# Optimization experiments

Hardware: AMD Instinct MI355X
Metric: run time of the kernel (lower is better)

Reference implementation:

```python
import jax, jax.numpy as jnp
import numpy as np

B, N, C, H, D, CS, CZ = 2, 512, 768, 16, 48, 384, 128  # batch, tokens, c_token, heads, head_dim, c_s, c_pair


def _ln(x, w=None, b=None, eps=1e-5):
    m = jnp.mean(x, axis=-1, keepdims=True)
    v = jnp.mean(jnp.square(x - m), axis=-1, keepdims=True)
    y = (x - m) * jax.lax.rsqrt(v + eps)
    if w is not None:
        y = y * w
    if b is not None:
        y = y + b
    return y


def setup_inputs() -> dict:
    key = jax.random.key(0)
    ks = jax.random.split(key, 16)
    s = 0.02
    return {
        "a_i": jax.random.normal(ks[0], (B, N, C), jnp.float32),
        "s_i": jax.random.normal(ks[1], (B, N, CS), jnp.float32),
        "z_ij": jax.random.normal(ks[2], (B, N, N, CZ), jnp.float32),
        "beta_ij": jax.random.normal(ks[3], (B, N, N), jnp.float32),
        # MHA projections (CustomAttention: q has bias; k, v, g, o have no bias)
        "Wq": jax.random.normal(ks[4], (C, C), jnp.float32) * s,
        "bq": jnp.zeros((C,), jnp.float32),
        "Wk": jax.random.normal(ks[5], (C, C), jnp.float32) * s,
        "Wv": jax.random.normal(ks[6], (C, C), jnp.float32) * s,
        "Wg": jax.random.normal(ks[7], (C, C), jnp.float32) * s,
        "Wo": jax.random.normal(ks[8], (C, C), jnp.float32) * s,
        # AdaLN: LN1 no affine; LN2 weight only; linear (bias) + linear_no_bias
        "ada_ln2_w": jnp.ones((CS,), jnp.float32),
        "ada_Wl": jax.random.normal(ks[9], (C, CS), jnp.float32) * s,
        "ada_bl": jnp.zeros((C,), jnp.float32),
        "ada_Wnb": jax.random.normal(ks[10], (C, CS), jnp.float32) * s,
        # pair-bias path
        "lnz_w": jnp.ones((CZ,), jnp.float32),
        "lnz_b": jnp.zeros((CZ,), jnp.float32),
        "Wz": jax.random.normal(ks[11], (H, CZ), jnp.float32) * s,
        # output gating from s_i (bias initialized to -2.0)
        "Wgs": jax.random.normal(ks[12], (C, CS), jnp.float32) * s,
        "bgs": jnp.full((C,), -2.0, jnp.float32),
    }


def reference(a_i, s_i, z_ij, beta_ij, Wq, bq, Wk, Wv, Wg, Wo,
              ada_ln2_w, ada_Wl, ada_bl, ada_Wnb, lnz_w, lnz_b, Wz, Wgs, bgs):
    b, n, c = a_i.shape
    # AdaLN conditioning
    a = _ln(a_i)                                   # [B,N,C], no affine
    s = _ln(s_i, ada_ln2_w)                        # [B,N,CS], weight only
    a = jax.nn.sigmoid(s @ ada_Wl.T + ada_bl) * a + s @ ada_Wnb.T
    # pair bias: LN(z) -> per-head logits -> [B,H,N,N]
    zb = _ln(z_ij, lnz_w, lnz_b) @ Wz.T            # [B,N,N,H]
    bias = jnp.transpose(zb, (0, 3, 1, 2)) + beta_ij[:, None, :, :]
    # multi-head attention with additive bias
    q = (a @ Wq.T + bq).reshape(b, n, H, D) / jnp.sqrt(jnp.asarray(D, a.dtype))
    k = (a @ Wk.T).reshape(b, n, H, D)
    v = (a @ Wv.T).reshape(b, n, H, D)
    scores = jnp.einsum("bqhd,bkhd->bhqk", q, k) + bias
    attn = jax.nn.softmax(scores, axis=-1)
    o = jnp.einsum("bhqk,bkhd->bqhd", attn, v)     # [B,N,H,D]
    g = jax.nn.sigmoid((a @ Wg.T).reshape(b, n, H, D))
    o = (g * o).reshape(b, n, c) @ Wo.T
    # final gating from raw s_i
    return jax.nn.sigmoid(s_i @ Wgs.T + bgs) * o
```

## Files before the change

kernel.cpp:

```cpp
#include <hip/hip_runtime.h>
#include <hip/hip_bf16.h>

#define NB 2
#define NN 512
#define CC 768
#define NH 16
#define DD 48
#define CS 384
#define CZ 128

__device__ inline float2 wave_reduce_sum2(float s, float q) {
  #pragma unroll
  for (int off = 32; off > 0; off >>= 1) {
    s += __shfl_xor(s, off);
    q += __shfl_xor(q, off);
  }
  return make_float2(s, q);
}

__device__ inline float sigmoidf_(float x) { return 1.f / (1.f + __expf(-x)); }

__global__ __launch_bounds__(256) void k_ln(
    const float* __restrict__ a_i, const float* __restrict__ s_i,
    const float* __restrict__ ln2w,
    float* __restrict__ aln, float* __restrict__ sln) {
  int r = blockIdx.x, t = threadIdx.x;
  int lane = t & 63, w = t >> 6;
  __shared__ float red[2][4];

  const float* ar = a_i + (size_t)r * CC;
  float x0 = ar[t], x1 = ar[t + 256], x2 = ar[t + 512];
  float s = x0 + x1 + x2, sq = x0 * x0 + x1 * x1 + x2 * x2;
  float2 rs = wave_reduce_sum2(s, sq);
  if (lane == 0) { red[0][w] = rs.x; red[1][w] = rs.y; }
  __syncthreads();
  float S = red[0][0] + red[0][1] + red[0][2] + red[0][3];
  float SQ = red[1][0] + red[1][1] + red[1][2] + red[1][3];
  float mean = S * (1.f / CC);
  float var = SQ * (1.f / CC) - mean * mean;
  float rstd = rsqrtf(var + 1e-5f);
  float* alr = aln + (size_t)r * CC;
  alr[t] = (x0 - mean) * rstd;
  alr[t + 256] = (x1 - mean) * rstd;
  alr[t + 512] = (x2 - mean) * rstd;

  const float* sr = s_i + (size_t)r * CS;
  float y0 = sr[t];
  float y1 = (t < 128) ? sr[256 + t] : 0.f;
  float s2 = y0 + y1, sq2 = y0 * y0 + y1 * y1;
  float2 rs2 = wave_reduce_sum2(s2, sq2);
  __syncthreads();
  if (lane == 0) { red[0][w] = rs2.x; red[1][w] = rs2.y; }
  __syncthreads();
  float S2 = red[0][0] + red[0][1] + red[0][2] + red[0][3];
  float SQ2 = red[1][0] + red[1][1] + red[1][2] + red[1][3];
  float mean2 = S2 * (1.f / CS);
  float var2 = SQ2 * (1.f / CS) - mean2 * mean2;
  float rstd2 = rsqrtf(var2 + 1e-5f);
  float* slr = sln + (size_t)r * CS;
  slr[t] = (y0 - mean2) * rstd2 * ln2w[t];
  if (t < 128) slr[256 + t] = (y1 - mean2) * rstd2 * ln2w[256 + t];
}

__global__ __launch_bounds__(256) void k_adaln(
    const float* __restrict__ sln, const float* __restrict__ aln,
    const float* __restrict__ Wl, const float* __restrict__ bl,
    const float* __restrict__ Wnb, float* __restrict__ acond) {
  __shared__ __align__(16) float As[16][36], B1[16][68], B2[16][68];
  int cb = blockIdx.x * 64, rb = blockIdx.y * 32;
  int t = threadIdx.x, tr = t >> 4, tc = t & 15;
  int lk = t & 15, lr = t >> 4;
  float acc1[2][4] = {}, acc2[2][4] = {};
  for (int kb = 0; kb < CS; kb += 16) {
    #pragma unroll
    for (int i = 0; i < 2; ++i) {
      int row = lr + i * 16;
      As[lk][row] = sln[(size_t)(rb + row) * CS + kb + lk];
    }
    #pragma unroll
    for (int i = 0; i < 4; ++i) {
      int row = lr + i * 16;
      B1[lk][row] = Wl[(size_t)(cb + row) * CS + kb + lk];
      B2[lk][row] = Wnb[(size_t)(cb + row) * CS + kb + lk];
    }
    __syncthreads();
    #pragma unroll
    for (int k = 0; k < 16; ++k) {
      float2 av = ((const float2*)&As[k][0])[tr];
      float4 b1v = ((const float4*)&B1[k][0])[tc];
      float4 b2v = ((const float4*)&B2[k][0])[tc];
      float a[2] = {av.x, av.y};
      float b1a[4] = {b1v.x, b1v.y, b1v.z, b1v.w};
      float b2a[4] = {b2v.x, b2v.y, b2v.z, b2v.w};
      #pragma unroll
      for (int i = 0; i < 2; ++i)
        #pragma unroll
        for (int j = 0; j < 4; ++j) {
          acc1[i][j] += a[i] * b1a[j];
          acc2[i][j] += a[i] * b2a[j];
        }
    }
    __syncthreads();
  }
  #pragma unroll
  for (int i = 0; i < 2; ++i) {
    int r = rb + tr * 2 + i;
    #pragma unroll
    for (int j = 0; j < 4; ++j) {
      int c = cb + tc * 4 + j;
      float sig = sigmoidf_(acc1[i][j] + bl[c]);
      acond[(size_t)r * CC + c] = sig * aln[(size_t)r * CC + c] + acc2[i][j];
    }
  }
}

__global__ __launch_bounds__(256) void k_qkvg(
    const float* __restrict__ acond,
    const float* __restrict__ Wq, const float* __restrict__ bq,
    const float* __restrict__ Wk, const float* __restrict__ Wv,
    const float* __restrict__ Wg,
    float* __restrict__ qo, float* __restrict__ ko,
    float* __restrict__ vo, float* __restrict__ go) {
  __shared__ __align__(16) float As[16][68], Bs[16][68];
  int zid = blockIdx.z;
  const float* W = (zid == 0) ? Wq : (zid == 1) ? Wk : (zid == 2) ? Wv : Wg;
  int cb = blockIdx.x * 64, rb = blockIdx.y * 64;
  int t = threadIdx.x, tr = t >> 4, tc = t & 15;
  int lk = t & 15, lr = t >> 4;
  float acc[4][4] = {};
  for (int kb = 0; kb < CC; kb += 16) {
    #pragma unroll
    for (int i = 0; i < 4; ++i) {
      int row = lr + i * 16;
      As[lk][row] = acond[(size_t)(rb + row) * CC + kb + lk];
      Bs[lk][row] = W[(size_t)(cb + row) * CC + kb + lk];
    }
    __syncthreads();
    #pragma unroll
    for (int k = 0; k < 16; ++k) {
      float4 av = ((const float4*)&As[k][0])[tr];
      float4 bv = ((const float4*)&Bs[k][0])[tc];
      float a[4] = {av.x, av.y, av.z, av.w};
      float bb[4] = {bv.x, bv.y, bv.z, bv.w};
      #pragma unroll
      for (int i = 0; i < 4; ++i)
        #pragma unroll
        for (int j = 0; j < 4; ++j) acc[i][j] += a[i] * bb[j];
    }
    __syncthreads();
  }
  const float qscale = 0.14433756729740643f;
  #pragma unroll
  for (int i = 0; i < 4; ++i) {
    int r = rb + tr * 4 + i;
    #pragma unroll
    for (int j = 0; j < 4; ++j) {
      int c = cb + tc * 4 + j;
      size_t o = (size_t)r * CC + c;
      if (zid == 0)      qo[o] = (acc[i][j] + bq[c]) * qscale;
      else if (zid == 1) ko[o] = acc[i][j];
      else if (zid == 2) vo[o] = acc[i][j];
      else               go[o] = sigmoidf_(acc[i][j]);
    }
  }
}

__global__ __launch_bounds__(256) void k_wzprep(
    const float* __restrict__ lnzw, const float* __restrict__ lnzb,
    const float* __restrict__ Wz, float* __restrict__ Wzp,
    float* __restrict__ TK) {
  int t = threadIdx.x;
  for (int idx = t; idx < NH * CZ; idx += 256)
    Wzp[idx] = lnzw[idx & (CZ - 1)] * Wz[idx];
  if (t < 32) {
    int h = t & 15;
    const float* wr = Wz + (size_t)h * CZ;
    const float* coef = (t < 16) ? lnzw : lnzb;
    float acc = 0.f;
    for (int c = 0; c < CZ; ++c) acc += coef[c] * wr[c];
    TK[(t < 16) ? h : 16 + h] = acc;
  }
}

__global__ __launch_bounds__(256) void k_pairbias(
    const float* __restrict__ z, const float* __restrict__ beta,
    const float* __restrict__ Wzp, const float* __restrict__ TK,
    float* __restrict__ bias) {
  __shared__ __align__(16) float zs[256 * 32];
  int blk = blockIdx.x;
  int jh = blk & 1, i = (blk >> 1) & (NN - 1), b = blk >> 10;
  int t = threadIdx.x;
  int j = jh * 256 + t;

  const float* zbase = z + ((size_t)(b * NN + i) * NN + jh * 256) * CZ;
  const float4* Wzp4 = (const float4*)Wzp;
  float S[16];
  #pragma unroll
  for (int h = 0; h < 16; ++h) S[h] = 0.f;
  float sum = 0.f, sq = 0.f;

  int srow = t >> 3;
  int ss = t & 7;

  for (int ch = 0; ch < 4; ++ch) {
    __syncthreads();
    #pragma unroll
    for (int p = 0; p < 8; ++p) {
      int r = p * 32 + srow;
      float4 v = *(const float4*)(zbase + (size_t)r * CZ + ch * 32 + ss * 4);
      *(float4*)&zs[r * 32 + ((ss ^ (r & 7)) << 2)] = v;
    }
    __syncthreads();
    #pragma unroll
    for (int s = 0; s < 8; ++s) {
      float4 zv = *(const float4*)&zs[t * 32 + ((s ^ (t & 7)) << 2)];
      sum += (zv.x + zv.y) + (zv.z + zv.w);
      sq += zv.x * zv.x + zv.y * zv.y + zv.z * zv.z + zv.w * zv.w;
      #pragma unroll
      for (int h = 0; h < 16; ++h) {
        float4 wv = Wzp4[h * 32 + ch * 8 + s];
        S[h] += zv.x * wv.x + zv.y * wv.y + zv.z * wv.z + zv.w * wv.w;
      }
    }
  }
  float mean = sum * (1.f / CZ);
  float var = fmaxf(sq * (1.f / CZ) - mean * mean, 0.f);
  float rstd = rsqrtf(var + 1e-5f);
  float bet = beta[((size_t)(b * NN + i)) * NN + j];
  size_t obase = (((size_t)b * NH) * NN + i) * NN + j;
  #pragma unroll
  for (int h = 0; h < 16; ++h) {
    bias[obase + (size_t)h * NN * NN] =
        rstd * (S[h] - mean * TK[h]) + TK[16 + h] + bet;
  }
}

__global__ __launch_bounds__(256) void k_attn(
    const float* __restrict__ q, const float* __restrict__ k,
    const float* __restrict__ v, const float* __restrict__ g,
    const float* __restrict__ bias, float* __restrict__ go_out) {
  __shared__ __align__(16) float qs[32][49];
  __shared__ __align__(16) float ks[64][49];
  __shared__ __align__(16) float vs[64][49];
  __shared__ __align__(16) float ps[32][65];
  __shared__ __align__(16) float bs[32][65];
  __shared__ float mrow[32], lrow[32], crow[32];
  int blk = blockIdx.x;
  int it = blk & 15, h = (blk >> 4) & 15, b = blk >> 8;
  int ibase = it * 32;
  int t = threadIdx.x;
  int tr = t >> 4, tc = t & 15;
  int td = t & 15;
  int sr = t >> 3, sl = t & 7;

  for (int idx = t; idx < 32 * 48; idx += 256) {
    int r = idx / 48, c = idx % 48;
    qs[r][c] = q[((size_t)(b * NN) + ibase + r) * CC + h * DD + c];
  }
  if (t < 32) { mrow[t] = -1e30f; lrow[t] = 0.f; }
  float acc[2][3] = {};
  const size_t bh = (size_t)b * NH + h;

  for (int jb = 0; jb < NN; jb += 64) {
    __syncthreads();
    for (int idx = t; idx < 64 * 48; idx += 256) {
      int r = idx / 48, c = idx % 48;
      size_t src = ((size_t)(b * NN) + jb + r) * CC + h * DD + c;
      ks[r][c] = k[src];
      vs[r][c] = v[src];
    }
    for (int idx = t; idx < 32 * 64; idx += 256) {
      int r = idx >> 6, c = idx & 63;
      bs[r][c] = bias[(bh * NN + ibase + r) * NN + jb + c];
    }
    __syncthreads();
    float sc[2][4] = {};
    #pragma unroll
    for (int d = 0; d < DD; ++d) {
      float a0 = qs[tr * 2][d], a1 = qs[tr * 2 + 1][d];
      #pragma unroll
      for (int j = 0; j < 4; ++j) {
        float bk = ks[tc * 4 + j][d];
        sc[0][j] += a0 * bk;
        sc[1][j] += a1 * bk;
      }
    }
    #pragma unroll
    for (int i = 0; i < 2; ++i)
      #pragma unroll
      for (int j = 0; j < 4; ++j)
        ps[tr * 2 + i][tc * 4 + j] = sc[i][j] + bs[tr * 2 + i][tc * 4 + j];
    __syncthreads();
    {
      float lm = -1e30f;
      #pragma unroll
      for (int jj = 0; jj < 8; ++jj) lm = fmaxf(lm, ps[sr][sl * 8 + jj]);
      lm = fmaxf(lm, __shfl_xor(lm, 1));
      lm = fmaxf(lm, __shfl_xor(lm, 2));
      lm = fmaxf(lm, __shfl_xor(lm, 4));
      float m_old = mrow[sr];
      float rmax = fmaxf(m_old, lm);
      float lsum = 0.f;
      #pragma unroll
      for (int jj = 0; jj < 8; ++jj) {
        float p = __expf(ps[sr][sl * 8 + jj] - rmax);
        ps[sr][sl * 8 + jj] = p;
        lsum += p;
      }
      lsum += __shfl_xor(lsum, 1);
      lsum += __shfl_xor(lsum, 2);
      lsum += __shfl_xor(lsum, 4);
      if (sl == 0) {
        float corr = __expf(m_old - rmax);
        lrow[sr] = lrow[sr] * corr + lsum;
        mrow[sr] = rmax;
        crow[sr] = corr;
      }
    }
    __syncthreads();
    float c0 = crow[tr * 2], c1 = crow[tr * 2 + 1];
    #pragma unroll
    for (int dd = 0; dd < 3; ++dd) { acc[0][dd] *= c0; acc[1][dd] *= c1; }
    #pragma unroll
    for (int ji = 0; ji < 64; ++ji) {
      float p0 = ps[tr * 2][ji], p1 = ps[tr * 2 + 1][ji];
      #pragma unroll
      for (int dd = 0; dd < 3; ++dd) {
        float vv = vs[ji][td * 3 + dd];
        acc[0][dd] += p0 * vv;
        acc[1][dd] += p1 * vv;
      }
    }
  }
  __syncthreads();
  #pragma unroll
  for (int i = 0; i < 2; ++i) {
    int qi = tr * 2 + i;
    float inv = 1.f / lrow[qi];
    #pragma unroll
    for (int dd = 0; dd < 3; ++dd) {
      int d = td * 3 + dd;
      size_t o = ((size_t)(b * NN) + ibase + qi) * CC + h * DD + d;
      go_out[o] = acc[i][dd] * inv * g[o];
    }
  }
}

__global__ __launch_bounds__(256) void k_out(
    const float* __restrict__ go, const float* __restrict__ Wo,
    const float* __restrict__ s_i, const float* __restrict__ Wgs,
    const float* __restrict__ bgs, float* __restrict__ out) {
  __shared__ __align__(16) float As[16][36], Bs[16][68];
  int cb = blockIdx.x * 64, rb = blockIdx.y * 32;
  int t = threadIdx.x, tr = t >> 4, tc = t & 15;
  int lk = t & 15, lr = t >> 4;
  float acc1[2][4] = {}, acc2[2][4] = {};
  for (int kb = 0; kb < CC; kb += 16) {
    #pragma unroll
    for (int i = 0; i < 2; ++i) {
      int row = lr + i * 16;
      As[lk][row] = go[(size_t)(rb + row) * CC + kb + lk];
    }
    #pragma unroll
    for (int i = 0; i < 4; ++i) {
      int row = lr + i * 16;
      Bs[lk][row] = Wo[(size_t)(cb + row) * CC + kb + lk];
    }
    __syncthreads();
    #pragma unroll
    for (int k = 0; k < 16; ++k) {
      float2 av = ((const float2*)&As[k][0])[tr];
      float4 bv = ((const float4*)&Bs[k][0])[tc];
      float a[2] = {av.x, av.y};
      float bb[4] = {bv.x, bv.y, bv.z, bv.w};
      #pragma unroll
      for (int i = 0; i < 2; ++i)
        #pragma unroll
        for (int j = 0; j < 4; ++j) acc1[i][j] += a[i] * bb[j];
    }
    __syncthreads();
  }
  for (int kb = 0; kb < CS; kb += 16) {
    #pragma unroll
    for (int i = 0; i < 2; ++i) {
      int row = lr + i * 16;
      As[lk][row] = s_i[(size_t)(rb + row) * CS + kb + lk];
    }
    #pragma unroll
    for (int i = 0; i < 4; ++i) {
      int row = lr + i * 16;
      Bs[lk][row] = Wgs[(size_t)(cb + row) * CS + kb + lk];
    }
    __syncthreads();
    #pragma unroll
    for (int k = 0; k < 16; ++k) {
      float2 av = ((const float2*)&As[k][0])[tr];
      float4 bv = ((const float4*)&Bs[k][0])[tc];
      float a[2] = {av.x, av.y};
      float bb[4] = {bv.x, bv.y, bv.z, bv.w};
      #pragma unroll
      for (int i = 0; i < 2; ++i)
        #pragma unroll
        for (int j = 0; j < 4; ++j) acc2[i][j] += a[i] * bb[j];
    }
    __syncthreads();
  }
  #pragma unroll
  for (int i = 0; i < 2; ++i) {
    int r = rb + tr * 2 + i;
    #pragma unroll
    for (int j = 0; j < 4; ++j) {
      int c = cb + tc * 4 + j;
      float gate = sigmoidf_(acc2[i][j] + bgs[c]);
      out[(size_t)r * CC + c] = gate * acc1[i][j];
    }
  }
}

extern "C" void kernel_launch(void* const* d_in, const int* in_sizes, int n_in,
                              void* d_out, int out_size, void* d_ws, size_t ws_size,
                              hipStream_t stream) {
  const float* a_i  = (const float*)d_in[0];
  const float* s_i  = (const float*)d_in[1];
  const float* z_ij = (const float*)d_in[2];
  const float* beta = (const float*)d_in[3];
  const float* Wq   = (const float*)d_in[4];
  const float* bq   = (const float*)d_in[5];
  const float* Wk   = (const float*)d_in[6];
  const float* Wv   = (const float*)d_in[7];
  const float* Wg   = (const float*)d_in[8];
  const float* Wo   = (const float*)d_in[9];
  const float* ada_ln2_w = (const float*)d_in[10];
  const float* ada_Wl = (const float*)d_in[11];
  const float* ada_bl = (const float*)d_in[12];
  const float* ada_Wnb = (const float*)d_in[13];
  const float* lnz_w = (const float*)d_in[14];
  const float* lnz_b = (const float*)d_in[15];
  const float* Wz  = (const float*)d_in[16];
  const float* Wgs = (const float*)d_in[17];
  const float* bgs = (const float*)d_in[18];
  float* out = (float*)d_out;

  float* ws = (float*)d_ws;
  const size_t RC = (size_t)NB * NN * CC;
  const size_t RS = (size_t)NB * NN * CS;
  float* aln   = ws;
  float* sln   = aln + RC;
  float* acond = sln + RS;
  float* qb    = acond + RC;
  float* kb    = qb + RC;
  float* vb    = kb + RC;
  float* gb    = vb + RC;
  float* gob   = gb + RC;
  float* biasb = gob + RC;
  float* Wzp   = biasb + (size_t)NB * NH * NN * NN;
  float* TK    = Wzp + NH * CZ;

  k_ln<<<NB * NN, 256, 0, stream>>>(a_i, s_i, ada_ln2_w, aln, sln);
  k_wzprep<<<1, 256, 0, stream>>>(lnz_w, lnz_b, Wz, Wzp, TK);
  k_adaln<<<dim3(CC / 64, NB * NN / 32), 256, 0, stream>>>(
      sln, aln, ada_Wl, ada_bl, ada_Wnb, acond);
  k_pairbias<<<NB * NN * (NN / 256), 256, 0, stream>>>(
      z_ij, beta, Wzp, TK, biasb);
  k_qkvg<<<dim3(CC / 64, NB * NN / 64, 4), 256, 0, stream>>>(
      acond, Wq, bq, Wk, Wv, Wg, qb, kb, vb, gb);
  k_attn<<<NB * NH * (NN / 32), 256, 0, stream>>>(qb, kb, vb, gb, biasb, gob);
  k_out<<<dim3(CC / 64, NB * NN / 32), 256, 0, stream>>>(
      gob, Wo, s_i, Wgs, bgs, out);
}
```

Measured before the change: 740.5 us.

## Register-tile pair-bias projection with shared weights and transposed z tile

Rewrites the pair-bias kernel so each thread computes a 4-row by 4-head tile of outputs from a transposed z tile and an LDS copy of the folded weights. Before, each thread did one row against all 16 heads and reloaded the weights from global memory. Per-row LayerNorm statistics are now gathered during the global load and reduced with shuffles. Outputs are written as float4 vectors. This raises arithmetic intensity and reduces weight-load traffic, at the cost of scalar transposed LDS stores that may bank-conflict.

```diff
diff --git a/kernel.cpp b/kernel.cpp
--- a/kernel.cpp
+++ b/kernel.cpp
@@ -186,52 +186,99 @@
     const float* __restrict__ z, const float* __restrict__ beta,
     const float* __restrict__ Wzp, const float* __restrict__ TK,
     float* __restrict__ bias) {
-  __shared__ __align__(16) float zs[256 * 32];
+  __shared__ __align__(16) float zs[32][260];
+  __shared__ __align__(16) float ws[128][20];
+  __shared__ float rowstat[256][2];
+  __shared__ float tks[32];
   int blk = blockIdx.x;
   int jh = blk & 1, i = (blk >> 1) & (NN - 1), b = blk >> 10;
   int t = threadIdx.x;
-  int j = jh * 256 + t;
-
-  const float* zbase = z + ((size_t)(b * NN + i) * NN + jh * 256) * CZ;
-  const float4* Wzp4 = (const float4*)Wzp;
-  float S[16];
-  #pragma unroll
-  for (int h = 0; h < 16; ++h) S[h] = 0.f;
-  float sum = 0.f, sq = 0.f;
-
+  int jbase = jh * 256;
+
+  {
+    int h = t >> 4, c0 = (t & 15) * 8;
+    float4 w0 = *(const float4*)(Wzp + (size_t)h * CZ + c0);
+    float4 w1 = *(const float4*)(Wzp + (size_t)h * CZ + c0 + 4);
+    ws[c0 + 0][h] = w0.x; ws[c0 + 1][h] = w0.y;
+    ws[c0 + 2][h] = w0.z; ws[c0 + 3][h] = w0.w;
+    ws[c0 + 4][h] = w1.x; ws[c0 + 5][h] = w1.y;
+    ws[c0 + 6][h] = w1.z; ws[c0 + 7][h] = w1.w;
+  }
+  if (t < 32) tks[t] = TK[t];
+
+  const float* zb = z + ((size_t)(b * NN + i) * NN + jbase) * CZ;
   int srow = t >> 3;
-  int ss = t & 7;
+  int sc = (t & 7) * 4;
+  int rg = t >> 2;
+  int hg = t & 3;
+
+  float acc[4][4] = {};
+  float ssum[8] = {}, ssq[8] = {};
 
   for (int ch = 0; ch < 4; ++ch) {
     __syncthreads();
     #pragma unroll
     for (int p = 0; p < 8; ++p) {
       int r = p * 32 + srow;
-      float4 v = *(const float4*)(zbase + (size_t)r * CZ + ch * 32 + ss * 4);
-      *(float4*)&zs[r * 32 + ((ss ^ (r & 7)) << 2)] = v;
-    }
-    __syncthreads();
-    #pragma unroll
-    for (int s = 0; s < 8; ++s) {
-      float4 zv = *(const float4*)&zs[t * 32 + ((s ^ (t & 7)) << 2)];
-      sum += (zv.x + zv.y) + (zv.z + zv.w);
-      sq += zv.x * zv.x + zv.y * zv.y + zv.z * zv.z + zv.w * zv.w;
-      #pragma unroll
-      for (int h = 0; h < 16; ++h) {
-        float4 wv = Wzp4[h * 32 + ch * 8 + s];
-        S[h] += zv.x * wv.x + zv.y * wv.y + zv.z * wv.z + zv.w * wv.w;
-      }
-    }
-  }
-  float mean = sum * (1.f / CZ);
-  float var = fmaxf(sq * (1.f / CZ) - mean * mean, 0.f);
-  float rstd = rsqrtf(var + 1e-5f);
-  float bet = beta[((size_t)(b * NN + i)) * NN + j];
-  size_t obase = (((size_t)b * NH) * NN + i) * NN + j;
-  #pragma unroll
-  for (int h = 0; h < 16; ++h) {
-    bias[obase + (size_t)h * NN * NN] =
-        rstd * (S[h] - mean * TK[h]) + TK[16 + h] + bet;
+      float4 v = *(const float4*)(zb + (size_t)r * CZ + ch * 32 + sc);
+      zs[sc + 0][r] = v.x; zs[sc + 1][r] = v.y;
+      zs[sc + 2][r] = v.z; zs[sc + 3][r] = v.w;
+      ssum[p] += (v.x + v.y) + (v.z + v.w);
+      ssq[p] += v.x * v.x + v.y * v.y + v.z * v.z + v.w * v.w;
+    }
+    __syncthreads();
+    #pragma unroll
+    for (int c = 0; c < 32; ++c) {
+      float4 zv = *(const float4*)&zs[c][rg * 4];
+      float4 wv = *(const float4*)&ws[ch * 32 + c][hg * 4];
+      float za[4] = {zv.x, zv.y, zv.z, zv.w};
+      float wa[4] = {wv.x, wv.y, wv.z, wv.w};
+      #pragma unroll
+      for (int ri = 0; ri < 4; ++ri)
+        #pragma unroll
+        for (int hi = 0; hi < 4; ++hi) acc[ri][hi] += za[ri] * wa[hi];
+    }
+  }
+
+  #pragma unroll
+  for (int p = 0; p < 8; ++p) {
+    ssum[p] += __shfl_xor(ssum[p], 1);
+    ssum[p] += __shfl_xor(ssum[p], 2);
+    ssum[p] += __shfl_xor(ssum[p], 4);
+    ssq[p] += __shfl_xor(ssq[p], 1);
+    ssq[p] += __shfl_xor(ssq[p], 2);
+    ssq[p] += __shfl_xor(ssq[p], 4);
+  }
+  if ((t & 7) == 0) {
+    #pragma unroll
+    for (int p = 0; p < 8; ++p) {
+      rowstat[p * 32 + srow][0] = ssum[p];
+      rowstat[p * 32 + srow][1] = ssq[p];
+    }
+  }
+  __syncthreads();
+
+  float4 bv = *(const float4*)(beta + ((size_t)(b * NN + i)) * NN + jbase + rg * 4);
+  float betv[4] = {bv.x, bv.y, bv.z, bv.w};
+  float mean[4], rstd[4];
+  #pragma unroll
+  for (int ri = 0; ri < 4; ++ri) {
+    float s = rowstat[rg * 4 + ri][0], q = rowstat[rg * 4 + ri][1];
+    mean[ri] = s * (1.f / CZ);
+    float var = fmaxf(q * (1.f / CZ) - mean[ri] * mean[ri], 0.f);
+    rstd[ri] = rsqrtf(var + 1e-5f);
+  }
+  size_t base = (((size_t)b * NH) * NN + i) * NN + jbase + rg * 4;
+  #pragma unroll
+  for (int hi = 0; hi < 4; ++hi) {
+    int h = hg * 4 + hi;
+    float tkh = tks[h], tkb = tks[16 + h];
+    float4 o;
+    o.x = rstd[0] * (acc[0][hi] - mean[0] * tkh) + tkb + betv[0];
+    o.y = rstd[1] * (acc[1][hi] - mean[1] * tkh) + tkb + betv[1];
+    o.z = rstd[2] * (acc[2][hi] - mean[2] * tkh) + tkb + betv[2];
+    o.w = rstd[3] * (acc[3][hi] - mean[3] * tkh) + tkb + betv[3];
+    *(float4*)(bias + base + (size_t)h * NN * NN) = o;
   }
 }
 
```

Result: faster. 681.6 us (-8.0%).
